# Kernel optimization log

Hardware: AMD Instinct MI355X
Metric: run time of the kernel (lower is better)

## Reference

```python
import jax, jax.numpy as jnp
import numpy as np

N = 100000
E = 1600000
C_IN = 32
HEADS = 4
C = 32          # per-head out channels
L = 3           # num layers = num_hidden_layers + 1
NEG_SLOPE = 0.2


def setup_inputs() -> dict:
    key = jax.random.key(0)
    ks = jax.random.split(key, 8)
    x = jax.random.normal(ks[0], (N, C_IN), dtype=jnp.float32)
    edge_index = jax.random.randint(ks[1], (2, E), 0, N, dtype=jnp.int64)
    edge_attr = jax.random.normal(ks[2], (E, 8), dtype=jnp.float32)  # unused by GATConv (edge_dim=None)
    scale = 1.0 / np.sqrt(C_IN)
    Ws = jax.random.normal(ks[3], (L, C_IN, HEADS * C), dtype=jnp.float32) * scale
    att_src = jax.random.normal(ks[4], (L, HEADS, C), dtype=jnp.float32) * scale
    att_dst = jax.random.normal(ks[5], (L, HEADS, C), dtype=jnp.float32) * scale
    bias = jnp.zeros((L, C), dtype=jnp.float32)
    return {"x": x, "edge_index": edge_index, "edge_attr": edge_attr,
            "Ws": Ws, "att_src": att_src, "att_dst": att_dst, "bias": bias}


def _gat_layer(x, src, dst, W, a_src, a_dst, b):
    # x: [N, C_in]; src/dst: [E'] (self-loops included); W: [C_in, H*C]
    h = (x @ W).reshape(N, HEADS, C)                      # [N, H, C]
    alpha_src = jnp.sum(h * a_src, axis=-1)               # [N, H]
    alpha_dst = jnp.sum(h * a_dst, axis=-1)               # [N, H]
    e = alpha_src[src] + alpha_dst[dst]                   # [E', H]
    e = jnp.where(e > 0, e, NEG_SLOPE * e)                # leaky_relu
    # segment softmax over incoming edges of each dst node
    m = jax.ops.segment_max(e, dst, num_segments=N)       # [N, H]
    ex = jnp.exp(e - m[dst])
    s = jax.ops.segment_sum(ex, dst, num_segments=N)      # [N, H]
    alpha = ex / (s[dst] + 1e-16)                         # [E', H]
    msg = h[src] * alpha[:, :, None]                      # [E', H, C]
    out = jax.ops.segment_sum(msg, dst, num_segments=N)   # [N, H, C]
    return out.mean(axis=1) + b                           # concat=False -> mean over heads, + bias


def reference(x, edge_index, edge_attr, Ws, att_src, att_dst, bias):
    # add self loops once (GATConv add_self_loops=True)
    loops = jnp.arange(N, dtype=edge_index.dtype)
    src = jnp.concatenate([edge_index[0], loops])
    dst = jnp.concatenate([edge_index[1], loops])
    # edge_attr unused: GATConv built without edge_dim.
    # Dropout layers are identity in eval mode.
    for l in range(L):
        x = _gat_layer(x, src, dst, Ws[l], att_src[l], att_dst[l], bias[l])
        x = jax.nn.elu(x)
    return x
```

## Files before the change

kernel.cpp:

```cpp
#include <hip/hip_runtime.h>
#include <hip/hip_bf16.h>
#include <hip/hip_fp16.h>
#include <cstdint>


__global__ void k_scan1(const int* __restrict__ deg, int n, int* __restrict__ bsums) {
    __shared__ int s[256];
    int t = threadIdx.x;
    int i = blockIdx.x * 256 + t;
    int v = (i < n) ? deg[i] : 0;
    s[t] = v; __syncthreads();
    for (int off = 128; off > 0; off >>= 1) {
        if (t < off) s[t] += s[t + off];
        __syncthreads();
    }
    if (t == 0) bsums[blockIdx.x] = s[0];
}

__global__ void k_scan2(const int* __restrict__ bsums, int nb, int* __restrict__ boffs) {
    __shared__ int s[512];
    int t = threadIdx.x;
    int v = (t < nb) ? bsums[t] : 0;
    s[t] = v; __syncthreads();
    for (int off = 1; off < 512; off <<= 1) {
        int nv = (t >= off) ? s[t - off] : 0;
        __syncthreads();
        s[t] += nv;
        __syncthreads();
    }
    if (t < nb) boffs[t] = s[t] - v;
}

__global__ void k_scan3(const int* __restrict__ deg, int n, const int* __restrict__ boffs,
                        int* __restrict__ rowst, int* __restrict__ cursor) {
    __shared__ int s[256];
    int t = threadIdx.x;
    int i = blockIdx.x * 256 + t;
    int v = (i < n) ? deg[i] : 0;
    s[t] = v; __syncthreads();
    for (int off = 1; off < 256; off <<= 1) {
        int nv = (t >= off) ? s[t - off] : 0;
        __syncthreads();
        s[t] += nv;
        __syncthreads();
    }
    int incl = s[t] + boffs[blockIdx.x];
    if (i < n) {
        int ex = incl - v;
        rowst[i] = ex;
        cursor[i] = ex;
        if (i == n - 1) rowst[n] = incl;
    }
}

__global__ void k_scatter(const int* __restrict__ src, const int* __restrict__ dst, int E,
                          int* __restrict__ cursor, int* __restrict__ col) {
    int t = blockIdx.x * blockDim.x + threadIdx.x;
    int base = t * 16;
    if (base + 16 <= E) {
        int4 d[4], s[4];
#pragma unroll
        for (int k = 0; k < 4; ++k) {
            d[k] = *reinterpret_cast<const int4*>(dst + base + k * 4);
            s[k] = *reinterpret_cast<const int4*>(src + base + k * 4);
        }
        const int* dd = reinterpret_cast<const int*>(d);
        const int* ss = reinterpret_cast<const int*>(s);
        int p[16];
#pragma unroll
        for (int k = 0; k < 16; ++k) p[k] = atomicAdd(&cursor[dd[k]], 1);
#pragma unroll
        for (int k = 0; k < 16; ++k) col[p[k]] = ss[k];
    } else {
        for (int i = base; i < E; ++i) {
            int p = atomicAdd(&cursor[dst[i]], 1);
            col[p] = src[i];
        }
    }
}


__device__ __forceinline__ float lane_bcast(float v, int k) {
    return __int_as_float(__builtin_amdgcn_readlane(__float_as_int(v), k));
}

__global__ void __launch_bounds__(256)
k_gemm_alpha(const float* __restrict__ x, const float* __restrict__ W,
             const float* __restrict__ a_src, const float* __restrict__ a_dst,
             __half* __restrict__ h16, float* __restrict__ alpha_src,
             float* __restrict__ alpha_dst, int n,
             const int* __restrict__ dstv, int E, int* __restrict__ deg,
             int gemmBlocks) {
    if ((int)blockIdx.x >= gemmBlocks) {
        int b = blockIdx.x - gemmBlocks;
        int base = (b * 256 + threadIdx.x) * 16;
        if (base + 16 <= E) {
            int4 d[4];
#pragma unroll
            for (int k = 0; k < 4; ++k)
                d[k] = *reinterpret_cast<const int4*>(dstv + base + k * 4);
            const int* dd = reinterpret_cast<const int*>(d);
#pragma unroll
            for (int k = 0; k < 16; ++k) atomicAdd(&deg[dd[k]], 1);
        } else {
            for (int i = base; i < E; ++i) atomicAdd(&deg[dstv[i]], 1);
        }
        return;
    }
    int lane = threadIdx.x & 63;
    int wave = threadIdx.x >> 6;
    int j2 = lane * 2;
    int nbase = blockIdx.x * 64 + wave * 16;

    float2 wr[32];
#pragma unroll
    for (int k = 0; k < 32; ++k)
        wr[k] = *reinterpret_cast<const float2*>(W + k * 128 + j2);
    float2 as2 = *reinterpret_cast<const float2*>(a_src + j2);
    float2 ad2 = *reinterpret_cast<const float2*>(a_dst + j2);

    float xr[16];
#pragma unroll
    for (int m = 0; m < 16; ++m) {
        int node = nbase + m;
        xr[m] = (node < n) ? x[(size_t)node * 32 + (lane & 31)] : 0.f;
    }

#pragma unroll
    for (int m = 0; m < 16; ++m) {
        int node = nbase + m;
        if (node >= n) continue;
        float acc0 = 0.f, acc1 = 0.f;
#pragma unroll
        for (int k = 0; k < 32; ++k) {
            float xv = lane_bcast(xr[m], k);
            acc0 += xv * wr[k].x;
            acc1 += xv * wr[k].y;
        }
        *reinterpret_cast<__half2*>(h16 + (size_t)node * 128 + j2) =
            __floats2half2_rn(acc0, acc1);
        float ps = acc0 * as2.x + acc1 * as2.y;
        float pd = acc0 * ad2.x + acc1 * ad2.y;
#pragma unroll
        for (int mm = 1; mm < 16; mm <<= 1) {
            ps += __shfl_xor(ps, mm, 64);
            pd += __shfl_xor(pd, mm, 64);
        }
        if ((lane & 15) == 0) {
            int head = lane >> 4;
            alpha_src[node * 4 + head] = ps;
            alpha_dst[node * 4 + head] = pd;
        }
    }
}

__device__ __forceinline__ float lrelu_exp(float e) {
    e = e > 0.f ? e : 0.2f * e;
    return __expf(e);
}

__device__ __forceinline__ float4 h16_to_f4(uint2 v) {
    float2 fa = __half22float2(*reinterpret_cast<__half2*>(&v.x));
    float2 fb = __half22float2(*reinterpret_cast<__half2*>(&v.y));
    return make_float4(fa.x, fa.y, fb.x, fb.y);
}

__global__ void k_agg(const __half* __restrict__ h16, const float* __restrict__ asrc,
                      const float* __restrict__ adst, const int* __restrict__ rowst,
                      const int* __restrict__ col, const float* __restrict__ bias,
                      float* __restrict__ out, int n) {
    int wid = (int)((blockIdx.x * (size_t)blockDim.x + threadIdx.x) >> 6);
    if (wid >= n) return;
    int lane = threadIdx.x & 63;
    int half = lane >> 5;
    int q = lane & 31;
    int head = q >> 3;
    float ad = adst[wid * 4 + head];

    float4 acc = make_float4(0.f, 0.f, 0.f, 0.f);
    float s = 0.f;
    if (half == 0) {
        float w = lrelu_exp(asrc[wid * 4 + head] + ad);
        uint2 v = *reinterpret_cast<const uint2*>(h16 + (size_t)wid * 128 + q * 4);
        float4 hv = h16_to_f4(v);
        s = w;
        acc.x = w * hv.x; acc.y = w * hv.y; acc.z = w * hv.z; acc.w = w * hv.w;
    }

    int beg = rowst[wid], end = rowst[wid + 1];
    int i = beg;
    for (; i + 8 <= end; i += 8) {
        int base = i + half * 4;
        int s0 = col[base], s1 = col[base + 1], s2 = col[base + 2], s3 = col[base + 3];
        float x0 = asrc[s0 * 4 + head];
        float x1 = asrc[s1 * 4 + head];
        float x2 = asrc[s2 * 4 + head];
        float x3 = asrc[s3 * 4 + head];
        uint2 v0 = *reinterpret_cast<const uint2*>(h16 + (size_t)s0 * 128 + q * 4);
        uint2 v1 = *reinterpret_cast<const uint2*>(h16 + (size_t)s1 * 128 + q * 4);
        uint2 v2 = *reinterpret_cast<const uint2*>(h16 + (size_t)s2 * 128 + q * 4);
        uint2 v3 = *reinterpret_cast<const uint2*>(h16 + (size_t)s3 * 128 + q * 4);
        float w0 = lrelu_exp(x0 + ad);
        float w1 = lrelu_exp(x1 + ad);
        float w2 = lrelu_exp(x2 + ad);
        float w3 = lrelu_exp(x3 + ad);
        float4 h0 = h16_to_f4(v0), h1 = h16_to_f4(v1), h2 = h16_to_f4(v2), h3 = h16_to_f4(v3);
        s += w0 + w1 + w2 + w3;
        acc.x += w0 * h0.x + w1 * h1.x + w2 * h2.x + w3 * h3.x;
        acc.y += w0 * h0.y + w1 * h1.y + w2 * h2.y + w3 * h3.y;
        acc.z += w0 * h0.z + w1 * h1.z + w2 * h2.z + w3 * h3.z;
        acc.w += w0 * h0.w + w1 * h1.w + w2 * h2.w + w3 * h3.w;
    }
    for (; i + 2 <= end; i += 2) {
        int sidx = col[i + half];
        float w = lrelu_exp(asrc[sidx * 4 + head] + ad);
        float4 hv = h16_to_f4(*reinterpret_cast<const uint2*>(h16 + (size_t)sidx * 128 + q * 4));
        s += w;
        acc.x += w * hv.x; acc.y += w * hv.y; acc.z += w * hv.z; acc.w += w * hv.w;
    }
    if (i < end && half == 0) {
        int sidx = col[i];
        float w = lrelu_exp(asrc[sidx * 4 + head] + ad);
        float4 hv = h16_to_f4(*reinterpret_cast<const uint2*>(h16 + (size_t)sidx * 128 + q * 4));
        s += w;
        acc.x += w * hv.x; acc.y += w * hv.y; acc.z += w * hv.z; acc.w += w * hv.w;
    }

    s += __shfl_xor(s, 32, 64);
    acc.x += __shfl_xor(acc.x, 32, 64);
    acc.y += __shfl_xor(acc.y, 32, 64);
    acc.z += __shfl_xor(acc.z, 32, 64);
    acc.w += __shfl_xor(acc.w, 32, 64);
    float inv = 1.f / s;
    acc.x *= inv; acc.y *= inv; acc.z *= inv; acc.w *= inv;
    acc.x += __shfl_xor(acc.x, 8, 64);  acc.x += __shfl_xor(acc.x, 16, 64);
    acc.y += __shfl_xor(acc.y, 8, 64);  acc.y += __shfl_xor(acc.y, 16, 64);
    acc.z += __shfl_xor(acc.z, 8, 64);  acc.z += __shfl_xor(acc.z, 16, 64);
    acc.w += __shfl_xor(acc.w, 8, 64);  acc.w += __shfl_xor(acc.w, 16, 64);
    if (lane < 8) {
        float4 b4 = *reinterpret_cast<const float4*>(&bias[lane * 4]);
        float o0 = acc.x * 0.25f + b4.x;
        float o1 = acc.y * 0.25f + b4.y;
        float o2 = acc.z * 0.25f + b4.z;
        float o3 = acc.w * 0.25f + b4.w;
        o0 = o0 > 0.f ? o0 : (__expf(o0) - 1.f);
        o1 = o1 > 0.f ? o1 : (__expf(o1) - 1.f);
        o2 = o2 > 0.f ? o2 : (__expf(o2) - 1.f);
        o3 = o3 > 0.f ? o3 : (__expf(o3) - 1.f);
        *reinterpret_cast<float4*>(&out[(size_t)wid * 32 + lane * 4]) =
            make_float4(o0, o1, o2, o3);
    }
}


extern "C" void kernel_launch(void* const* d_in, const int* in_sizes, int n_in,
                              void* d_out, int out_size, void* d_ws, size_t ws_size,
                              hipStream_t stream) {
    const float* x       = (const float*)d_in[0];
    const int*   ei      = (const int*)d_in[1];
    const float* Ws      = (const float*)d_in[3];
    const float* att_src = (const float*)d_in[4];
    const float* att_dst = (const float*)d_in[5];
    const float* bias    = (const float*)d_in[6];

    int N = in_sizes[0] / 32;
    int E = in_sizes[1] / 2;
    const int* srcv = ei;
    const int* dstv = ei + E;

    float* fws   = (float*)d_ws;
    __half* h16  = (__half*)fws;
    float* asrc  = (float*)(h16 + (size_t)N * 128);
    float* adst  = asrc + (size_t)N * 4;
    float* xbuf  = adst + (size_t)N * 4;
    int*   deg    = (int*)(xbuf + (size_t)N * 32);
    int*   rowst  = deg + N;
    int*   cursor = rowst + N + 1;
    int*   bsums  = cursor + N;
    int*   boffs  = bsums + 512;
    int*   col    = boffs + 512;

    int nb256 = (N + 255) / 256;
    int gemmBlocks = (N + 63) / 64;
    int histBlocks = (E + 16 * 256 - 1) / (16 * 256);
    int scatBlocks = (E + 16 * 256 - 1) / (16 * 256);

    hipMemsetAsync(deg, 0, (size_t)N * sizeof(int), stream);

    for (int l = 0; l < 3; ++l) {
        const float* xin = (l == 0) ? x : xbuf;
        float* xout = (l == 2) ? (float*)d_out : xbuf;
        int extra = (l == 0) ? histBlocks : 0;
        k_gemm_alpha<<<gemmBlocks + extra, 256, 0, stream>>>(
            xin, Ws + (size_t)l * 32 * 128, att_src + l * 128, att_dst + l * 128,
            h16, asrc, adst, N, dstv, E, deg, gemmBlocks);
        if (l == 0) {
            k_scan1<<<nb256, 256, 0, stream>>>(deg, N, bsums);
            k_scan2<<<1, 512, 0, stream>>>(bsums, nb256, boffs);
            k_scan3<<<nb256, 256, 0, stream>>>(deg, N, boffs, rowst, cursor);
            k_scatter<<<scatBlocks, 256, 0, stream>>>(srcv, dstv, E, cursor, col);
        }
        k_agg<<<(N + 3) / 4, 256, 0, stream>>>(
            h16, asrc, adst, rowst, col, bias + l * 32, xout, N);
    }
}
```

Measured before the change: 493.3 us.

## Record per-edge rank in histogram pass so CSR scatter needs no atomics

The degree histogram now saves the value returned by each atomicAdd as that edge's rank within its destination row. The scatter pass then computes the slot as row start plus rank, with no second round of atomics on a cursor array. This costs an extra E-sized int array written and read back. Edges per thread drop from 16 to 8 in both passes. Because ranks come from atomic order, neighbour order within a row is still non-deterministic, as before.

```diff
diff --git a/kernel.cpp b/kernel.cpp
--- a/kernel.cpp
+++ b/kernel.cpp
@@ -32,7 +32,7 @@
 }
 
 __global__ void k_scan3(const int* __restrict__ deg, int n, const int* __restrict__ boffs,
-                        int* __restrict__ rowst, int* __restrict__ cursor) {
+                        int* __restrict__ rowst) {
     __shared__ int s[256];
     int t = threadIdx.x;
     int i = blockIdx.x * 256 + t;
@@ -46,36 +46,34 @@
     }
     int incl = s[t] + boffs[blockIdx.x];
     if (i < n) {
-        int ex = incl - v;
-        rowst[i] = ex;
-        cursor[i] = ex;
+        rowst[i] = incl - v;
         if (i == n - 1) rowst[n] = incl;
     }
 }
 
-__global__ void k_scatter(const int* __restrict__ src, const int* __restrict__ dst, int E,
-                          int* __restrict__ cursor, int* __restrict__ col) {
+__global__ void k_scatter(const int* __restrict__ src, const int* __restrict__ dst,
+                          const int* __restrict__ rank, const int* __restrict__ rowst,
+                          int E, int* __restrict__ col) {
     int t = blockIdx.x * blockDim.x + threadIdx.x;
-    int base = t * 16;
-    if (base + 16 <= E) {
-        int4 d[4], s[4];
-#pragma unroll
-        for (int k = 0; k < 4; ++k) {
+    int base = t * 8;
+    if (base + 8 <= E) {
+        int4 d[2], s[2], r[2];
+#pragma unroll
+        for (int k = 0; k < 2; ++k) {
             d[k] = *reinterpret_cast<const int4*>(dst + base + k * 4);
             s[k] = *reinterpret_cast<const int4*>(src + base + k * 4);
+            r[k] = *reinterpret_cast<const int4*>(rank + base + k * 4);
         }
         const int* dd = reinterpret_cast<const int*>(d);
         const int* ss = reinterpret_cast<const int*>(s);
-        int p[16];
-#pragma unroll
-        for (int k = 0; k < 16; ++k) p[k] = atomicAdd(&cursor[dd[k]], 1);
-#pragma unroll
-        for (int k = 0; k < 16; ++k) col[p[k]] = ss[k];
+        const int* rr = reinterpret_cast<const int*>(r);
+        int p[8];
+#pragma unroll
+        for (int k = 0; k < 8; ++k) p[k] = rowst[dd[k]] + rr[k];
+#pragma unroll
+        for (int k = 0; k < 8; ++k) col[p[k]] = ss[k];
     } else {
-        for (int i = base; i < E; ++i) {
-            int p = atomicAdd(&cursor[dst[i]], 1);
-            col[p] = src[i];
-        }
+        for (int i = base; i < E; ++i) col[rowst[dst[i]] + rank[i]] = src[i];
     }
 }
 
@@ -90,20 +88,25 @@
              __half* __restrict__ h16, float* __restrict__ alpha_src,
              float* __restrict__ alpha_dst, int n,
              const int* __restrict__ dstv, int E, int* __restrict__ deg,
-             int gemmBlocks) {
+             int* __restrict__ rank, int gemmBlocks) {
     if ((int)blockIdx.x >= gemmBlocks) {
         int b = blockIdx.x - gemmBlocks;
-        int base = (b * 256 + threadIdx.x) * 16;
-        if (base + 16 <= E) {
-            int4 d[4];
-#pragma unroll
-            for (int k = 0; k < 4; ++k)
+        int base = (b * 256 + threadIdx.x) * 8;
+        if (base + 8 <= E) {
+            int4 d[2];
+#pragma unroll
+            for (int k = 0; k < 2; ++k)
                 d[k] = *reinterpret_cast<const int4*>(dstv + base + k * 4);
             const int* dd = reinterpret_cast<const int*>(d);
-#pragma unroll
-            for (int k = 0; k < 16; ++k) atomicAdd(&deg[dd[k]], 1);
+            int r[8];
+#pragma unroll
+            for (int k = 0; k < 8; ++k) r[k] = atomicAdd(&deg[dd[k]], 1);
+#pragma unroll
+            for (int k = 0; k < 2; ++k)
+                *reinterpret_cast<int4*>(rank + base + k * 4) =
+                    *reinterpret_cast<const int4*>(r + k * 4);
         } else {
-            for (int i = base; i < E; ++i) atomicAdd(&deg[dstv[i]], 1);
+            for (int i = base; i < E; ++i) rank[i] = atomicAdd(&deg[dstv[i]], 1);
         }
         return;
     }
@@ -275,30 +278,29 @@
     float* xbuf  = adst + (size_t)N * 4;
     int*   deg    = (int*)(xbuf + (size_t)N * 32);
     int*   rowst  = deg + N;
-    int*   cursor = rowst + N + 1;
-    int*   bsums  = cursor + N;
+    int*   bsums  = rowst + N + 1;
     int*   boffs  = bsums + 512;
     int*   col    = boffs + 512;
+    int*   rank   = col + E;
 
     int nb256 = (N + 255) / 256;
     int gemmBlocks = (N + 63) / 64;
-    int histBlocks = (E + 16 * 256 - 1) / (16 * 256);
-    int scatBlocks = (E + 16 * 256 - 1) / (16 * 256);
+    int edgeBlocks8 = (E + 8 * 256 - 1) / (8 * 256);
 
     hipMemsetAsync(deg, 0, (size_t)N * sizeof(int), stream);
 
     for (int l = 0; l < 3; ++l) {
         const float* xin = (l == 0) ? x : xbuf;
         float* xout = (l == 2) ? (float*)d_out : xbuf;
-        int extra = (l == 0) ? histBlocks : 0;
+        int extra = (l == 0) ? edgeBlocks8 : 0;
         k_gemm_alpha<<<gemmBlocks + extra, 256, 0, stream>>>(
             xin, Ws + (size_t)l * 32 * 128, att_src + l * 128, att_dst + l * 128,
-            h16, asrc, adst, N, dstv, E, deg, gemmBlocks);
+            h16, asrc, adst, N, dstv, E, deg, rank, gemmBlocks);
         if (l == 0) {
             k_scan1<<<nb256, 256, 0, stream>>>(deg, N, bsums);
             k_scan2<<<1, 512, 0, stream>>>(bsums, nb256, boffs);
-            k_scan3<<<nb256, 256, 0, stream>>>(deg, N, boffs, rowst, cursor);
-            k_scatter<<<scatBlocks, 256, 0, stream>>>(srcv, dstv, E, cursor, col);
+            k_scan3<<<nb256, 256, 0, stream>>>(deg, N, boffs, rowst);
+            k_scatter<<<edgeBlocks8, 256, 0, stream>>>(srcv, dstv, rank, rowst, E, col);
         }
         k_agg<<<(N + 3) / 4, 256, 0, stream>>>(
             h16, asrc, adst, rowst, col, bias + l * 32, xout, N);
```

After: 448.1 us. 1.1x faster.
